# Kernel optimization log

Hardware: AMD Instinct MI355X
Metric: run time of the kernel (lower is better)

The kernel has to match this reference:

```python
import jax, jax.numpy as jnp
import numpy as np

N, F_IN, H, C = 100000, 256, 128, 64
E, EP = 1600000, 500000


def setup_inputs() -> dict:
    key = jax.random.key(0)
    ks = jax.random.split(key, 8)
    x = jax.random.normal(ks[0], (N, F_IN), jnp.float32)
    masked_nodes = jax.random.randint(ks[1], (1000,), 0, N)
    pos_edge_index = jax.random.randint(ks[2], (2, EP), 0, N)
    neg_edge_index = jax.random.randint(ks[3], (2, EP), 0, N)
    edge_index = jax.random.randint(ks[4], (2, E), 0, N)
    W1 = jax.random.normal(ks[5], (F_IN, H), jnp.float32) / np.sqrt(F_IN).astype(np.float32)
    b1 = jnp.zeros((H,), jnp.float32)
    W2 = jax.random.normal(ks[6], (H, C), jnp.float32) / np.sqrt(H).astype(np.float32)
    b2 = jnp.zeros((C,), jnp.float32)
    return dict(x=x, masked_nodes=masked_nodes, pos_edge_index=pos_edge_index,
                neg_edge_index=neg_edge_index, edge_index=edge_index,
                W1=W1, b1=b1, W2=W2, b2=b2)


def gcn_conv(x, W, b, src, dst, n):
    # PyG GCNConv: h = x @ W; symmetric norm with self-loops; aggregate; + bias
    h = x @ W  # [N, out]
    deg = jax.ops.segment_sum(jnp.ones(src.shape[0], h.dtype), dst, num_segments=n) + 1.0
    dis = jax.lax.rsqrt(deg)  # D^{-1/2} including self-loop
    msg = h[src] * (dis[src] * dis[dst])[:, None]           # gather + edge-norm
    agg = jax.ops.segment_sum(msg, dst, num_segments=n)      # scatter-add
    agg = agg + h * (dis * dis)[:, None]                      # self-loop term
    return agg + b


def reference(x, masked_nodes, pos_edge_index, neg_edge_index, edge_index, W1, b1, W2, b2):
    n = x.shape[0]
    src, dst = edge_index[0], edge_index[1]
    h = jax.nn.relu(gcn_conv(x, W1, b1, src, dst, n))
    h = gcn_conv(h, W2, b2, src, dst, n)  # [N, C]
    tei = jnp.concatenate([pos_edge_index, neg_edge_index], axis=-1)  # [2, 2*EP]
    x_j = h[tei[0]]  # [2EP, C]
    x_i = h[tei[1]]
    scores = jnp.einsum('ef,ef->e', x_i, x_j)
    return scores, jnp.zeros(tei.shape, jnp.float32)
```

## Files before the change

kernel.cpp:

```cpp
#include <hip/hip_runtime.h>

#define N_NODES 100000
#define F_IN    256
#define H_DIM   128
#define C_DIM   64
#define E_EDGES 1600000
#define EP_EDGES 500000

#define NBUK 391
#define EPB  4096

typedef unsigned short bf16_t;
typedef short  short8  __attribute__((ext_vector_type(8)));
typedef float  float4v __attribute__((ext_vector_type(4)));
typedef _Float16 half8v __attribute__((ext_vector_type(8)));

__device__ inline bf16_t f2bf(float f) {
    unsigned u = __float_as_uint(f);
    u += 0x7fff + ((u >> 16) & 1);
    return (bf16_t)(u >> 16);
}
__device__ inline float bf2f(bf16_t h) {
    return __uint_as_float(((unsigned)h) << 16);
}
__device__ inline void split8(const float* vv, short* h, short* l) {
#pragma unroll
    for (int j = 0; j < 8; ++j) {
        bf16_t hb = f2bf(vv[j]);
        h[j] = (short)hb;
        l[j] = (short)f2bf(vv[j] - bf2f(hb));
    }
}
__device__ inline float4v mfma16(short8 a, short8 b, float4v c) {
    return __builtin_amdgcn_mfma_f32_16x16x32_bf16(a, b, c, 0, 0, 0);
}
__device__ inline void gload_lds16(const void* gptr, void* lptr) {
    __builtin_amdgcn_global_load_lds(
        (const __attribute__((address_space(1))) unsigned int*)gptr,
        (__attribute__((address_space(3))) unsigned int*)lptr, 16, 0, 0);
}
#define XSWZ(nn) (((nn) >> 1) & 3)

__global__ __launch_bounds__(256) void bhist_kernel(const int* __restrict__ dst,
                                                    int* __restrict__ bsize) {
    __shared__ int hist[NBUK];
    const int t = threadIdx.x;
    for (int b = t; b < NBUK; b += 256) hist[b] = 0;
    __syncthreads();
    const int e0 = blockIdx.x * EPB;
#pragma unroll
    for (int i = 0; i < 16; ++i) {
        int e = e0 + i * 256 + t;
        if (e < E_EDGES) atomicAdd(&hist[dst[e] >> 8], 1);
    }
    __syncthreads();
    for (int b = t; b < NBUK; b += 256)
        if (hist[b]) atomicAdd(&bsize[b], hist[b]);
}

__global__ __launch_bounds__(512) void bscan_kernel(const int* __restrict__ bsize,
                                                    int* __restrict__ bbase,
                                                    int* __restrict__ bcursor) {
    __shared__ int sh[512];
    int t = threadIdx.x;
    sh[t] = (t < NBUK) ? bsize[t] : 0;
    __syncthreads();
#pragma unroll
    for (int off = 1; off < 512; off <<= 1) {
        int u = (t >= off) ? sh[t - off] : 0;
        __syncthreads();
        sh[t] += u;
        __syncthreads();
    }
    if (t < NBUK) {
        int ex = (t == 0) ? 0 : sh[t - 1];
        bbase[t] = ex;
        bcursor[t] = ex;
    }
    if (t == 0) bbase[NBUK] = E_EDGES;
}

__global__ __launch_bounds__(256) void bucket_scatter_kernel(const int* __restrict__ src,
                                                             const int* __restrict__ dst,
                                                             int* __restrict__ bcursor,
                                                             int2* __restrict__ pairs) {
    __shared__ int hist[NBUK];
    __shared__ int base[NBUK];
    const int t = threadIdx.x;
    for (int b = t; b < NBUK; b += 256) hist[b] = 0;
    __syncthreads();

    const int e0 = blockIdx.x * EPB;
    int s[16], d[16];
#pragma unroll
    for (int i = 0; i < 16; ++i) {
        int e = e0 + i * 256 + t;
        if (e < E_EDGES) {
            s[i] = src[e];
            d[i] = dst[e];
            atomicAdd(&hist[d[i] >> 8], 1);
        } else {
            d[i] = -1;
        }
    }
    __syncthreads();
    for (int b = t; b < NBUK; b += 256) {
        int c = hist[b];
        base[b] = c ? atomicAdd(&bcursor[b], c) : 0;
        hist[b] = 0;
    }
    __syncthreads();
#pragma unroll
    for (int i = 0; i < 16; ++i) {
        if (d[i] >= 0) {
            int b = d[i] >> 8;
            int r = atomicAdd(&hist[b], 1);
            pairs[base[b] + r] = make_int2(s[i], d[i]);
        }
    }
}

__global__ __launch_bounds__(256) void bucket_sort_kernel(const int2* __restrict__ pairs,
                                                          const int* __restrict__ bbase,
                                                          int* __restrict__ row_ptr,
                                                          float* __restrict__ dis,
                                                          int* __restrict__ csr_src) {
    __shared__ int cnt[256];
    __shared__ int sh[256];
    __shared__ int cur[256];
    const int b = blockIdx.x;
    const int node0 = b << 8;
    const int t = threadIdx.x;
    const int nn = min(256, N_NODES - node0);
    const int beg = bbase[b], end = bbase[b + 1];
    cnt[t] = 0;
    __syncthreads();
    for (int e = beg + t; e < end; e += 256)
        atomicAdd(&cnt[pairs[e].y - node0], 1);
    __syncthreads();
    int c = cnt[t];
    if (t < nn) dis[node0 + t] = rsqrtf((float)c + 1.0f);
    sh[t] = c;
    __syncthreads();
#pragma unroll
    for (int off = 1; off < 256; off <<= 1) {
        int u = (t >= off) ? sh[t - off] : 0;
        __syncthreads();
        sh[t] += u;
        __syncthreads();
    }
    int start = beg + sh[t] - c;
    if (t < nn) row_ptr[node0 + t] = start;
    cur[t] = start;
    if (b == NBUK - 1 && t == 0) row_ptr[N_NODES] = E_EDGES;
    __syncthreads();
    for (int e = beg + t; e < end; e += 256) {
        int2 p = pairs[e];
        int j = atomicAdd(&cur[p.y - node0], 1);
        csr_src[j] = p.x;
    }
}

__global__ __launch_bounds__(256) void wprep_kernel(const float* __restrict__ W1,
                                                    const float* __restrict__ W2,
                                                    short* __restrict__ w1h,
                                                    short* __restrict__ w1l,
                                                    short* __restrict__ w2h,
                                                    short* __restrict__ w2l) {
    int idx = blockIdx.x * 256 + threadIdx.x;
    if (idx < H_DIM * F_IN) {
        int n = idx >> 8, k = idx & 255;
        int kc = (k >> 3) & 3;
        int dk = (k & ~0x18) | (((kc ^ XSWZ(n)) & 3) << 3);
        float w = W1[k * H_DIM + n];
        bf16_t h = f2bf(w);
        w1h[n * F_IN + dk] = (short)h;
        w1l[n * F_IN + dk] = (short)f2bf(w - bf2f(h));
    }
    int i2 = idx - H_DIM * F_IN;
    if (i2 >= 0 && i2 < C_DIM * H_DIM) {
        int n = i2 >> 7, k = i2 & 127;
        int kc = (k >> 3) & 3;
        int dk = (k & ~0x18) | (((kc ^ XSWZ(n)) & 3) << 3);
        float w = W2[k * C_DIM + n];
        bf16_t h = f2bf(w);
        w2h[n * H_DIM + dk] = (short)h;
        w2l[n * H_DIM + dk] = (short)f2bf(w - bf2f(h));
    }
}

#define G1_STAGE(BUF, KSN)                                                     \
    for (int i_ = 0; i_ < 2; ++i_) {                                           \
        int e_ = t + i_ * 256;                                                 \
        gload_lds16(&Wth[(e_ >> 2) * F_IN + (KSN) * 32 + (e_ & 3) * 8],        \
                    &Bh[(BUF) * 4096 + e_ * 8]);                               \
        gload_lds16(&Wtl[(e_ >> 2) * F_IN + (KSN) * 32 + (e_ & 3) * 8],        \
                    &Bl[(BUF) * 4096 + e_ * 8]);                               \
    }

#define G1_LOADA(BANK, KSN)                                                    \
    if (ok0) {                                                                 \
        *(float4*)&aP[BANK][0][0] = *(const float4*)&X0[(KSN) * 32];           \
        *(float4*)&aP[BANK][0][4] = *(const float4*)&X0[(KSN) * 32 + 4];       \
    }                                                                          \
    if (ok1) {                                                                 \
        *(float4*)&aP[BANK][1][0] = *(const float4*)&X1[(KSN) * 32];           \
        *(float4*)&aP[BANK][1][4] = *(const float4*)&X1[(KSN) * 32 + 4];       \
    }

__global__ __launch_bounds__(256, 3) void gemm1_mfma(const float* __restrict__ X,
                                                     const short* __restrict__ Wth,
                                                     const short* __restrict__ Wtl,
                                                     const float* __restrict__ dis,
                                                     bf16_t* __restrict__ T,
                                                     int nrows) {
    __shared__ short Bh[2 * 4096], Bl[2 * 4096];
    const int t = threadIdx.x;
    const int row0 = blockIdx.x * 128;
    const int w = t >> 6;
    const int lane = t & 63;
    const int m = lane & 15;
    const int q = lane >> 4;
    const int qs = ((q ^ XSWZ(m)) & 3) << 3;

    const int r0 = row0 + w * 32 + m;
    const int r1 = r0 + 16;
    const bool ok0 = r0 < nrows;
    const bool ok1 = r1 < nrows;
    const float* X0 = X + (long long)r0 * F_IN + q * 8;
    const float* X1 = X + (long long)r1 * F_IN + q * 8;

    float4v acc[2][8];
#pragma unroll
    for (int i = 0; i < 2; ++i)
#pragma unroll
        for (int j = 0; j < 8; ++j) acc[i][j] = {0.f, 0.f, 0.f, 0.f};

    float aP[2][2][8] = {};

    G1_STAGE(0, 0)
    G1_LOADA(0, 0)
    __syncthreads();

#pragma unroll
    for (int ks = 0; ks < 8; ++ks) {
        const int p = ks & 1;
        if (ks < 7) {
            G1_STAGE(p ^ 1, ks + 1)
            G1_LOADA(p ^ 1, ks + 1)
        }
        short8 ah0, al0, ah1, al1;
        split8(aP[p][0], (short*)&ah0, (short*)&al0);
        split8(aP[p][1], (short*)&ah1, (short*)&al1);
#pragma unroll
        for (int nc = 0; nc < 8; ++nc) {
            const int bo = p * 4096 + (nc * 16 + m) * 32 + qs;
            short8 bh = *(const short8*)&Bh[bo];
            short8 bl = *(const short8*)&Bl[bo];
            acc[0][nc] = mfma16(ah0, bh, acc[0][nc]);
            acc[0][nc] = mfma16(al0, bh, acc[0][nc]);
            acc[0][nc] = mfma16(ah0, bl, acc[0][nc]);
            acc[1][nc] = mfma16(ah1, bh, acc[1][nc]);
            acc[1][nc] = mfma16(al1, bh, acc[1][nc]);
            acc[1][nc] = mfma16(ah1, bl, acc[1][nc]);
        }
        __syncthreads();
    }
    float ds_[2][4];
#pragma unroll
    for (int mt = 0; mt < 2; ++mt)
#pragma unroll
        for (int reg = 0; reg < 4; ++reg) {
            int grow = row0 + w * 32 + mt * 16 + q * 4 + reg;
            ds_[mt][reg] = (grow < nrows) ? dis[grow] : 0.f;
        }
#pragma unroll
    for (int mt = 0; mt < 2; ++mt)
#pragma unroll
        for (int nc = 0; nc < 8; ++nc)
#pragma unroll
            for (int reg = 0; reg < 4; ++reg) {
                int grow = row0 + w * 32 + mt * 16 + q * 4 + reg;
                int gcol = nc * 16 + m;
                if (grow < nrows)
                    T[(long long)grow * H_DIM + gcol] = f2bf(acc[mt][nc][reg] * ds_[mt][reg]);
            }
}

#define G2_STAGE(BUF, KSN)                                                     \
    gload_lds16(&Wth[(t >> 2) * H_DIM + (KSN) * 32 + (t & 3) * 8],             \
                &Bh[(BUF) * 2048 + t * 8]);                                    \
    gload_lds16(&Wtl[(t >> 2) * H_DIM + (KSN) * 32 + (t & 3) * 8],             \
                &Bl[(BUF) * 2048 + t * 8]);

#define G2_LOADA(BANK, KSN)                                                    \
    if (ok0) {                                                                 \
        *(float4*)&aP[BANK][0][0] = *(const float4*)&A0[(KSN) * 32];           \
        *(float4*)&aP[BANK][0][4] = *(const float4*)&A0[(KSN) * 32 + 4];       \
    }                                                                          \
    if (ok1) {                                                                 \
        *(float4*)&aP[BANK][1][0] = *(const float4*)&A1[(KSN) * 32];           \
        *(float4*)&aP[BANK][1][4] = *(const float4*)&A1[(KSN) * 32 + 4];       \
    }

__global__ __launch_bounds__(256, 3) void gemm2_mfma(const float* __restrict__ A,
                                                     const float* __restrict__ b1,
                                                     const short* __restrict__ Wth,
                                                     const short* __restrict__ Wtl,
                                                     const float* __restrict__ dis,
                                                     bf16_t* __restrict__ T,
                                                     int nrows) {
    __shared__ short Bh[2 * 2048], Bl[2 * 2048];
    const int t = threadIdx.x;
    const int row0 = blockIdx.x * 128;
    const int w = t >> 6;
    const int lane = t & 63;
    const int m = lane & 15;
    const int q = lane >> 4;
    const int qs = ((q ^ XSWZ(m)) & 3) << 3;

    const int r0 = row0 + w * 32 + m;
    const int r1 = r0 + 16;
    const bool ok0 = r0 < nrows;
    const bool ok1 = r1 < nrows;
    const float* A0 = A + (long long)r0 * H_DIM + q * 8;
    const float* A1 = A + (long long)r1 * H_DIM + q * 8;
    const float* bp = b1 + q * 8;

    float4v acc[2][4];
#pragma unroll
    for (int i = 0; i < 2; ++i)
#pragma unroll
        for (int j = 0; j < 4; ++j) acc[i][j] = {0.f, 0.f, 0.f, 0.f};

    float aP[2][2][8] = {};

    G2_STAGE(0, 0)
    G2_LOADA(0, 0)
    __syncthreads();

#pragma unroll
    for (int ks = 0; ks < 4; ++ks) {
        const int p = ks & 1;
        if (ks < 3) {
            G2_STAGE(p ^ 1, ks + 1)
            G2_LOADA(p ^ 1, ks + 1)
        }
        float4 bv0 = *(const float4*)&bp[ks * 32];
        float4 bv1 = *(const float4*)&bp[ks * 32 + 4];
        float a0[8], a1[8];
        a0[0] = fmaxf(aP[p][0][0] + bv0.x, 0.f); a0[1] = fmaxf(aP[p][0][1] + bv0.y, 0.f);
        a0[2] = fmaxf(aP[p][0][2] + bv0.z, 0.f); a0[3] = fmaxf(aP[p][0][3] + bv0.w, 0.f);
        a0[4] = fmaxf(aP[p][0][4] + bv1.x, 0.f); a0[5] = fmaxf(aP[p][0][5] + bv1.y, 0.f);
        a0[6] = fmaxf(aP[p][0][6] + bv1.z, 0.f); a0[7] = fmaxf(aP[p][0][7] + bv1.w, 0.f);
        a1[0] = fmaxf(aP[p][1][0] + bv0.x, 0.f); a1[1] = fmaxf(aP[p][1][1] + bv0.y, 0.f);
        a1[2] = fmaxf(aP[p][1][2] + bv0.z, 0.f); a1[3] = fmaxf(aP[p][1][3] + bv0.w, 0.f);
        a1[4] = fmaxf(aP[p][1][4] + bv1.x, 0.f); a1[5] = fmaxf(aP[p][1][5] + bv1.y, 0.f);
        a1[6] = fmaxf(aP[p][1][6] + bv1.z, 0.f); a1[7] = fmaxf(aP[p][1][7] + bv1.w, 0.f);
        short8 ah0, al0, ah1, al1;
        split8(a0, (short*)&ah0, (short*)&al0);
        split8(a1, (short*)&ah1, (short*)&al1);
#pragma unroll
        for (int nc = 0; nc < 4; ++nc) {
            const int bo = p * 2048 + (nc * 16 + m) * 32 + qs;
            short8 bh = *(const short8*)&Bh[bo];
            short8 bl = *(const short8*)&Bl[bo];
            acc[0][nc] = mfma16(ah0, bh, acc[0][nc]);
            acc[0][nc] = mfma16(al0, bh, acc[0][nc]);
            acc[0][nc] = mfma16(ah0, bl, acc[0][nc]);
            acc[1][nc] = mfma16(ah1, bh, acc[1][nc]);
            acc[1][nc] = mfma16(al1, bh, acc[1][nc]);
            acc[1][nc] = mfma16(ah1, bl, acc[1][nc]);
        }
        __syncthreads();
    }
    float ds_[2][4];
#pragma unroll
    for (int mt = 0; mt < 2; ++mt)
#pragma unroll
        for (int reg = 0; reg < 4; ++reg) {
            int grow = row0 + w * 32 + mt * 16 + q * 4 + reg;
            ds_[mt][reg] = (grow < nrows) ? dis[grow] : 0.f;
        }
#pragma unroll
    for (int mt = 0; mt < 2; ++mt)
#pragma unroll
        for (int nc = 0; nc < 4; ++nc)
#pragma unroll
            for (int reg = 0; reg < 4; ++reg) {
                int grow = row0 + w * 32 + mt * 16 + q * 4 + reg;
                int gcol = nc * 16 + m;
                if (grow < nrows)
                    T[(long long)grow * C_DIM + gcol] = f2bf(acc[mt][nc][reg] * ds_[mt][reg]);
            }
}

__device__ inline void add8_bf16(float* acc, uint4 u) {
#pragma unroll
    for (int p = 0; p < 4; ++p) {
        unsigned w = (&u.x)[p];
        acc[2 * p]     += __uint_as_float(w << 16);
        acc[2 * p + 1] += __uint_as_float(w & 0xffff0000u);
    }
}

template <int CS, bool HAS_BIAS, bool F16OUT>
__global__ __launch_bounds__(256) void agg_kernel(const bf16_t* __restrict__ t,
                                                  const float* __restrict__ dis,
                                                  const int* __restrict__ row_ptr,
                                                  const int* __restrict__ csr_src,
                                                  const float* __restrict__ bias,
                                                  float* __restrict__ aggf,
                                                  _Float16* __restrict__ aggh) {
    unsigned idx = blockIdx.x * 256u + threadIdx.x;
    if (idx >= (unsigned)(N_NODES << CS)) return;
    int node = idx >> CS;
    int q = idx & ((1 << CS) - 1);
    const uint4* tv = (const uint4*)t;
    int beg = row_ptr[node], end = row_ptr[node + 1];

    float acc[8];
    {
        uint4 u = tv[idx];
#pragma unroll
        for (int p = 0; p < 4; ++p) {
            unsigned w = (&u.x)[p];
            acc[2 * p]     = __uint_as_float(w << 16);
            acc[2 * p + 1] = __uint_as_float(w & 0xffff0000u);
        }
    }

    int j = beg;
    for (; j + 3 < end; j += 4) {
        int s0 = csr_src[j + 0], s1 = csr_src[j + 1];
        int s2 = csr_src[j + 2], s3 = csr_src[j + 3];
        uint4 u0 = tv[((unsigned)s0 << CS) + q];
        uint4 u1 = tv[((unsigned)s1 << CS) + q];
        uint4 u2 = tv[((unsigned)s2 << CS) + q];
        uint4 u3 = tv[((unsigned)s3 << CS) + q];
        add8_bf16(acc, u0);
        add8_bf16(acc, u1);
        add8_bf16(acc, u2);
        add8_bf16(acc, u3);
    }
    for (; j < end; ++j) {
        int s = csr_src[j];
        add8_bf16(acc, tv[((unsigned)s << CS) + q]);
    }

    float dd = dis[node];
#pragma unroll
    for (int p = 0; p < 8; ++p) acc[p] *= dd;

    if (HAS_BIAS) {
        float4 bv0 = ((const float4*)bias)[q * 2];
        float4 bv1 = ((const float4*)bias)[q * 2 + 1];
        acc[0] += bv0.x; acc[1] += bv0.y; acc[2] += bv0.z; acc[3] += bv0.w;
        acc[4] += bv1.x; acc[5] += bv1.y; acc[6] += bv1.z; acc[7] += bv1.w;
    }
    if (F16OUT) {
        half8v hv;
#pragma unroll
        for (int p = 0; p < 8; ++p) hv[p] = (_Float16)acc[p];
        ((half8v*)aggh)[idx] = hv;
    } else {
        float4 o0 = make_float4(acc[0], acc[1], acc[2], acc[3]);
        float4 o1 = make_float4(acc[4], acc[5], acc[6], acc[7]);
        ((float4*)aggf)[idx * 2]     = o0;
        ((float4*)aggf)[idx * 2 + 1] = o1;
    }
}

__global__ __launch_bounds__(256) void score_kernel(const _Float16* __restrict__ h2,
                                                    const int* __restrict__ pos,
                                                    const int* __restrict__ neg,
                                                    float* __restrict__ out) {
    int tid = blockIdx.x * 256 + threadIdx.x;
    int e = tid >> 3;
    int q = tid & 7;
    if (e >= 2 * EP_EDGES) return;
    int i, j;
    if (e < EP_EDGES) {
        j = pos[e];
        i = pos[EP_EDGES + e];
    } else {
        j = neg[e - EP_EDGES];
        i = neg[e];
    }
    half8v a = ((const half8v*)h2)[i * 8 + q];
    half8v b = ((const half8v*)h2)[j * 8 + q];
    float v = 0.f;
#pragma unroll
    for (int k = 0; k < 8; ++k) v = fmaf((float)a[k], (float)b[k], v);
    v += __shfl_down(v, 4, 8);
    v += __shfl_down(v, 2, 8);
    v += __shfl_down(v, 1, 8);
    if (q == 0) out[e] = v;
}

extern "C" void kernel_launch(void* const* d_in, const int* in_sizes, int n_in,
                              void* d_out, int out_size, void* d_ws, size_t ws_size,
                              hipStream_t stream) {
    const float* x  = (const float*)d_in[0];
    const int* pos  = (const int*)d_in[2];
    const int* neg  = (const int*)d_in[3];
    const int* ei   = (const int*)d_in[4];
    const float* W1 = (const float*)d_in[5];
    const float* b1 = (const float*)d_in[6];
    const float* W2 = (const float*)d_in[7];
    const float* b2 = (const float*)d_in[8];
    float* out = (float*)d_out;

    char* ws = (char*)d_ws;
    float*  dis     = (float*) (ws + 0);
    int*    row_ptr = (int*)   (ws + 400000);
    int*    bsize   = (int*)   (ws + 800128);
    int*    bbase   = (int*)   (ws + 801792);
    int*    bcursor = (int*)   (ws + 803456);
    int*    csr_src = (int*)   (ws + 805120);
    int2*   pairs   = (int2*)  (ws + 7205120);
    _Float16* h2f16 = (_Float16*)(ws + 7205120);
    bf16_t* t       = (bf16_t*)(ws + 20005120);
    float*  agg     = (float*) (ws + 45605120);
    short*  w1th    = (short*) (ws + 96805120);
    short*  w1tl    = (short*) (ws + 96870656);
    short*  w2th    = (short*) (ws + 96936192);
    short*  w2tl    = (short*) (ws + 96952576);

    const int* esrc = ei;
    const int* edst = ei + E_EDGES;

    hipMemsetAsync(bsize, 0, NBUK * sizeof(int), stream);
    bhist_kernel<<<(E_EDGES + EPB - 1) / EPB, 256, 0, stream>>>(edst, bsize);
    bscan_kernel<<<1, 512, 0, stream>>>(bsize, bbase, bcursor);
    bucket_scatter_kernel<<<(E_EDGES + EPB - 1) / EPB, 256, 0, stream>>>(
        esrc, edst, bcursor, pairs);
    bucket_sort_kernel<<<NBUK, 256, 0, stream>>>(pairs, bbase, row_ptr, dis, csr_src);
    wprep_kernel<<<(H_DIM * F_IN + C_DIM * H_DIM + 255) / 256, 256, 0, stream>>>(
        W1, W2, w1th, w1tl, w2th, w2tl);

    gemm1_mfma<<<(N_NODES + 127) / 128, 256, 0, stream>>>(x, w1th, w1tl, dis, t, N_NODES);
    agg_kernel<4, false, false><<<(N_NODES * 16 + 255) / 256, 256, 0, stream>>>(
        t, dis, row_ptr, csr_src, nullptr, agg, nullptr);

    gemm2_mfma<<<(N_NODES + 127) / 128, 256, 0, stream>>>(agg, b1, w2th, w2tl, dis, t, N_NODES);
    agg_kernel<3, true, true><<<(N_NODES * 8 + 255) / 256, 256, 0, stream>>>(
        t, dis, row_ptr, csr_src, b2, nullptr, h2f16);

    score_kernel<<<(2 * EP_EDGES * 8) / 256, 256, 0, stream>>>(h2f16, pos, neg, out);

    hipMemsetAsync(out + 2 * EP_EDGES, 0, (size_t)4 * EP_EDGES * sizeof(float), stream);
}
```

Measured before the change: 400.3 us.

## Pack bucket pairs into 32-bit words and use 512-thread gemm1 blocks

Bucket scatter now packs the source index and the low 8 bits of the destination into one 32-bit word instead of an int2. This halves the traffic for writing and reading pairs in the sort kernel. gemm1 now runs 512 threads per block, with each wave computing a 16-row tile instead of 32. That halves the accumulator and A-operand registers per thread to allow more resident waves, at the cost of less B-tile reuse per wave.

```diff
diff --git a/kernel.cpp b/kernel.cpp
--- a/kernel.cpp
+++ b/kernel.cpp
@@ -83,7 +83,7 @@
 __global__ __launch_bounds__(256) void bucket_scatter_kernel(const int* __restrict__ src,
                                                              const int* __restrict__ dst,
                                                              int* __restrict__ bcursor,
-                                                             int2* __restrict__ pairs) {
+                                                             unsigned* __restrict__ pairs) {
     __shared__ int hist[NBUK];
     __shared__ int base[NBUK];
     const int t = threadIdx.x;
@@ -115,12 +115,12 @@
         if (d[i] >= 0) {
             int b = d[i] >> 8;
             int r = atomicAdd(&hist[b], 1);
-            pairs[base[b] + r] = make_int2(s[i], d[i]);
-        }
-    }
-}
-
-__global__ __launch_bounds__(256) void bucket_sort_kernel(const int2* __restrict__ pairs,
+            pairs[base[b] + r] = ((unsigned)(d[i] & 255) << 24) | (unsigned)s[i];
+        }
+    }
+}
+
+__global__ __launch_bounds__(256) void bucket_sort_kernel(const unsigned* __restrict__ pairs,
                                                           const int* __restrict__ bbase,
                                                           int* __restrict__ row_ptr,
                                                           float* __restrict__ dis,
@@ -136,7 +136,7 @@
     cnt[t] = 0;
     __syncthreads();
     for (int e = beg + t; e < end; e += 256)
-        atomicAdd(&cnt[pairs[e].y - node0], 1);
+        atomicAdd(&cnt[pairs[e] >> 24], 1);
     __syncthreads();
     int c = cnt[t];
     if (t < nn) dis[node0 + t] = rsqrtf((float)c + 1.0f);
@@ -155,9 +155,9 @@
     if (b == NBUK - 1 && t == 0) row_ptr[N_NODES] = E_EDGES;
     __syncthreads();
     for (int e = beg + t; e < end; e += 256) {
-        int2 p = pairs[e];
-        int j = atomicAdd(&cur[p.y - node0], 1);
-        csr_src[j] = p.x;
+        unsigned p = pairs[e];
+        int j = atomicAdd(&cur[p >> 24], 1);
+        csr_src[j] = (int)(p & 0xFFFFFFu);
     }
 }
 
@@ -190,31 +190,24 @@
 }
 
 #define G1_STAGE(BUF, KSN)                                                     \
-    for (int i_ = 0; i_ < 2; ++i_) {                                           \
-        int e_ = t + i_ * 256;                                                 \
-        gload_lds16(&Wth[(e_ >> 2) * F_IN + (KSN) * 32 + (e_ & 3) * 8],        \
-                    &Bh[(BUF) * 4096 + e_ * 8]);                               \
-        gload_lds16(&Wtl[(e_ >> 2) * F_IN + (KSN) * 32 + (e_ & 3) * 8],        \
-                    &Bl[(BUF) * 4096 + e_ * 8]);                               \
-    }
+    gload_lds16(&Wth[(t >> 2) * F_IN + (KSN) * 32 + (t & 3) * 8],              \
+                &SB[(BUF) * 4096 + t * 8]);                                    \
+    gload_lds16(&Wtl[(t >> 2) * F_IN + (KSN) * 32 + (t & 3) * 8],              \
+                &SB[8192 + (BUF) * 4096 + t * 8]);
 
 #define G1_LOADA(BANK, KSN)                                                    \
     if (ok0) {                                                                 \
-        *(float4*)&aP[BANK][0][0] = *(const float4*)&X0[(KSN) * 32];           \
-        *(float4*)&aP[BANK][0][4] = *(const float4*)&X0[(KSN) * 32 + 4];       \
-    }                                                                          \
-    if (ok1) {                                                                 \
-        *(float4*)&aP[BANK][1][0] = *(const float4*)&X1[(KSN) * 32];           \
-        *(float4*)&aP[BANK][1][4] = *(const float4*)&X1[(KSN) * 32 + 4];       \
-    }
-
-__global__ __launch_bounds__(256, 3) void gemm1_mfma(const float* __restrict__ X,
+        *(float4*)&aP[BANK][0] = *(const float4*)&X0[(KSN) * 32];              \
+        *(float4*)&aP[BANK][4] = *(const float4*)&X0[(KSN) * 32 + 4];          \
+    }
+
+__global__ __launch_bounds__(512, 6) void gemm1_mfma(const float* __restrict__ X,
                                                      const short* __restrict__ Wth,
                                                      const short* __restrict__ Wtl,
                                                      const float* __restrict__ dis,
                                                      bf16_t* __restrict__ T,
                                                      int nrows) {
-    __shared__ short Bh[2 * 4096], Bl[2 * 4096];
+    __shared__ short SB[16384];
     const int t = threadIdx.x;
     const int row0 = blockIdx.x * 128;
     const int w = t >> 6;
@@ -223,20 +216,15 @@
     const int q = lane >> 4;
     const int qs = ((q ^ XSWZ(m)) & 3) << 3;
 
-    const int r0 = row0 + w * 32 + m;
-    const int r1 = r0 + 16;
+    const int r0 = row0 + w * 16 + m;
     const bool ok0 = r0 < nrows;
-    const bool ok1 = r1 < nrows;
     const float* X0 = X + (long long)r0 * F_IN + q * 8;
-    const float* X1 = X + (long long)r1 * F_IN + q * 8;
-
-    float4v acc[2][8];
-#pragma unroll
-    for (int i = 0; i < 2; ++i)
-#pragma unroll
-        for (int j = 0; j < 8; ++j) acc[i][j] = {0.f, 0.f, 0.f, 0.f};
-
-    float aP[2][2][8] = {};
+
+    float4v acc[8];
+#pragma unroll
+    for (int j = 0; j < 8; ++j) acc[j] = {0.f, 0.f, 0.f, 0.f};
+
+    float aP[2][8] = {};
 
     G1_STAGE(0, 0)
     G1_LOADA(0, 0)
@@ -249,42 +237,34 @@
             G1_STAGE(p ^ 1, ks + 1)
             G1_LOADA(p ^ 1, ks + 1)
         }
-        short8 ah0, al0, ah1, al1;
-        split8(aP[p][0], (short*)&ah0, (short*)&al0);
-        split8(aP[p][1], (short*)&ah1, (short*)&al1);
+        short8 ah0, al0;
+        split8(aP[p], (short*)&ah0, (short*)&al0);
 #pragma unroll
         for (int nc = 0; nc < 8; ++nc) {
             const int bo = p * 4096 + (nc * 16 + m) * 32 + qs;
-            short8 bh = *(const short8*)&Bh[bo];
-            short8 bl = *(const short8*)&Bl[bo];
-            acc[0][nc] = mfma16(ah0, bh, acc[0][nc]);
-            acc[0][nc] = mfma16(al0, bh, acc[0][nc]);
-            acc[0][nc] = mfma16(ah0, bl, acc[0][nc]);
-            acc[1][nc] = mfma16(ah1, bh, acc[1][nc]);
-            acc[1][nc] = mfma16(al1, bh, acc[1][nc]);
-            acc[1][nc] = mfma16(ah1, bl, acc[1][nc]);
+            short8 bh = *(const short8*)&SB[bo];
+            short8 bl = *(const short8*)&SB[8192 + bo];
+            acc[nc] = mfma16(ah0, bh, acc[nc]);
+            acc[nc] = mfma16(al0, bh, acc[nc]);
+            acc[nc] = mfma16(ah0, bl, acc[nc]);
         }
         __syncthreads();
     }
-    float ds_[2][4];
-#pragma unroll
-    for (int mt = 0; mt < 2; ++mt)
+    float ds_[4];
+#pragma unroll
+    for (int reg = 0; reg < 4; ++reg) {
+        int grow = row0 + w * 16 + q * 4 + reg;
+        ds_[reg] = (grow < nrows) ? dis[grow] : 0.f;
+    }
+#pragma unroll
+    for (int nc = 0; nc < 8; ++nc)
 #pragma unroll
         for (int reg = 0; reg < 4; ++reg) {
-            int grow = row0 + w * 32 + mt * 16 + q * 4 + reg;
-            ds_[mt][reg] = (grow < nrows) ? dis[grow] : 0.f;
-        }
-#pragma unroll
-    for (int mt = 0; mt < 2; ++mt)
-#pragma unroll
-        for (int nc = 0; nc < 8; ++nc)
-#pragma unroll
-            for (int reg = 0; reg < 4; ++reg) {
-                int grow = row0 + w * 32 + mt * 16 + q * 4 + reg;
-                int gcol = nc * 16 + m;
-                if (grow < nrows)
-                    T[(long long)grow * H_DIM + gcol] = f2bf(acc[mt][nc][reg] * ds_[mt][reg]);
-            }
+            int grow = row0 + w * 16 + q * 4 + reg;
+            int gcol = nc * 16 + m;
+            if (grow < nrows)
+                T[(long long)grow * H_DIM + gcol] = f2bf(acc[nc][reg] * ds_[reg]);
+        }
 }
 
 #define G2_STAGE(BUF, KSN)                                                     \
@@ -518,7 +498,7 @@
     int*    bbase   = (int*)   (ws + 801792);
     int*    bcursor = (int*)   (ws + 803456);
     int*    csr_src = (int*)   (ws + 805120);
-    int2*   pairs   = (int2*)  (ws + 7205120);
+    unsigned* pairs = (unsigned*)(ws + 7205120);
     _Float16* h2f16 = (_Float16*)(ws + 7205120);
     bf16_t* t       = (bf16_t*)(ws + 20005120);
     float*  agg     = (float*) (ws + 45605120);
@@ -539,7 +519,7 @@
     wprep_kernel<<<(H_DIM * F_IN + C_DIM * H_DIM + 255) / 256, 256, 0, stream>>>(
         W1, W2, w1th, w1tl, w2th, w2tl);
 
-    gemm1_mfma<<<(N_NODES + 127) / 128, 256, 0, stream>>>(x, w1th, w1tl, dis, t, N_NODES);
+    gemm1_mfma<<<(N_NODES + 127) / 128, 512, 0, stream>>>(x, w1th, w1tl, dis, t, N_NODES);
     agg_kernel<4, false, false><<<(N_NODES * 16 + 255) / 256, 256, 0, stream>>>(
         t, dis, row_ptr, csr_src, nullptr, agg, nullptr);
 
```

Result: no change. 404.4 us (+1.0%).

## Pack bucket pairs into 32-bit words and restage GEMM loads in bulk phases

Applied to the files above, without the earlier changes.

Bucket scatter now stores each edge as one 32-bit word, with the local destination in the high 8 bits and the source in the low 24 bits. This halves the traffic for writing and reading the intermediate pairs array. gemm1 switches from a per-k-step double buffer to two bulk phases: it loads half of the weights and all of the X row fragments into registers up front, which cuts barriers and lets more loads be in flight. In exchange it uses more LDS and registers, and launch bounds drop to 2 blocks per SM. gemm2 likewise loads all weights and A fragments before computing, with a single barrier.

```diff
diff --git a/kernel.cpp b/kernel.cpp
--- a/kernel.cpp
+++ b/kernel.cpp
@@ -83,7 +83,7 @@
 __global__ __launch_bounds__(256) void bucket_scatter_kernel(const int* __restrict__ src,
                                                              const int* __restrict__ dst,
                                                              int* __restrict__ bcursor,
-                                                             int2* __restrict__ pairs) {
+                                                             unsigned* __restrict__ pairs) {
     __shared__ int hist[NBUK];
     __shared__ int base[NBUK];
     const int t = threadIdx.x;
@@ -115,12 +115,12 @@
         if (d[i] >= 0) {
             int b = d[i] >> 8;
             int r = atomicAdd(&hist[b], 1);
-            pairs[base[b] + r] = make_int2(s[i], d[i]);
-        }
-    }
-}
-
-__global__ __launch_bounds__(256) void bucket_sort_kernel(const int2* __restrict__ pairs,
+            pairs[base[b] + r] = ((unsigned)(d[i] & 255) << 24) | (unsigned)s[i];
+        }
+    }
+}
+
+__global__ __launch_bounds__(256) void bucket_sort_kernel(const unsigned* __restrict__ pairs,
                                                           const int* __restrict__ bbase,
                                                           int* __restrict__ row_ptr,
                                                           float* __restrict__ dis,
@@ -136,7 +136,7 @@
     cnt[t] = 0;
     __syncthreads();
     for (int e = beg + t; e < end; e += 256)
-        atomicAdd(&cnt[pairs[e].y - node0], 1);
+        atomicAdd(&cnt[pairs[e] >> 24], 1);
     __syncthreads();
     int c = cnt[t];
     if (t < nn) dis[node0 + t] = rsqrtf((float)c + 1.0f);
@@ -155,9 +155,9 @@
     if (b == NBUK - 1 && t == 0) row_ptr[N_NODES] = E_EDGES;
     __syncthreads();
     for (int e = beg + t; e < end; e += 256) {
-        int2 p = pairs[e];
-        int j = atomicAdd(&cur[p.y - node0], 1);
-        csr_src[j] = p.x;
+        unsigned p = pairs[e];
+        int j = atomicAdd(&cur[p >> 24], 1);
+        csr_src[j] = (int)(p & 0xFFFFFFu);
     }
 }
 
@@ -189,32 +189,13 @@
     }
 }
 
-#define G1_STAGE(BUF, KSN)                                                     \
-    for (int i_ = 0; i_ < 2; ++i_) {                                           \
-        int e_ = t + i_ * 256;                                                 \
-        gload_lds16(&Wth[(e_ >> 2) * F_IN + (KSN) * 32 + (e_ & 3) * 8],        \
-                    &Bh[(BUF) * 4096 + e_ * 8]);                               \
-        gload_lds16(&Wtl[(e_ >> 2) * F_IN + (KSN) * 32 + (e_ & 3) * 8],        \
-                    &Bl[(BUF) * 4096 + e_ * 8]);                               \
-    }
-
-#define G1_LOADA(BANK, KSN)                                                    \
-    if (ok0) {                                                                 \
-        *(float4*)&aP[BANK][0][0] = *(const float4*)&X0[(KSN) * 32];           \
-        *(float4*)&aP[BANK][0][4] = *(const float4*)&X0[(KSN) * 32 + 4];       \
-    }                                                                          \
-    if (ok1) {                                                                 \
-        *(float4*)&aP[BANK][1][0] = *(const float4*)&X1[(KSN) * 32];           \
-        *(float4*)&aP[BANK][1][4] = *(const float4*)&X1[(KSN) * 32 + 4];       \
-    }
-
-__global__ __launch_bounds__(256, 3) void gemm1_mfma(const float* __restrict__ X,
+__global__ __launch_bounds__(256, 2) void gemm1_mfma(const float* __restrict__ X,
                                                      const short* __restrict__ Wth,
                                                      const short* __restrict__ Wtl,
                                                      const float* __restrict__ dis,
                                                      bf16_t* __restrict__ T,
                                                      int nrows) {
-    __shared__ short Bh[2 * 4096], Bl[2 * 4096];
+    __shared__ short SB[32768];
     const int t = threadIdx.x;
     const int row0 = blockIdx.x * 128;
     const int w = t >> 6;
@@ -236,25 +217,182 @@
 #pragma unroll
         for (int j = 0; j < 8; ++j) acc[i][j] = {0.f, 0.f, 0.f, 0.f};
 
-    float aP[2][2][8] = {};
-
-    G1_STAGE(0, 0)
-    G1_LOADA(0, 0)
-    __syncthreads();
-
-#pragma unroll
-    for (int ks = 0; ks < 8; ++ks) {
-        const int p = ks & 1;
-        if (ks < 7) {
-            G1_STAGE(p ^ 1, ks + 1)
-            G1_LOADA(p ^ 1, ks + 1)
-        }
+    float aP[4][2][8] = {};
+    float aQ[4][2][8] = {};
+
+#pragma unroll
+    for (int pp = 0; pp < 4; ++pp)
+#pragma unroll
+        for (int i_ = 0; i_ < 2; ++i_) {
+            int e_ = t + i_ * 256;
+            gload_lds16(&Wth[(e_ >> 2) * F_IN + pp * 32 + (e_ & 3) * 8],
+                        &SB[pp * 4096 + e_ * 8]);
+            gload_lds16(&Wtl[(e_ >> 2) * F_IN + pp * 32 + (e_ & 3) * 8],
+                        &SB[16384 + pp * 4096 + e_ * 8]);
+        }
+    if (ok0)
+#pragma unroll
+        for (int pp = 0; pp < 4; ++pp) {
+            *(float4*)&aP[pp][0][0] = *(const float4*)&X0[pp * 32];
+            *(float4*)&aP[pp][0][4] = *(const float4*)&X0[pp * 32 + 4];
+            *(float4*)&aQ[pp][0][0] = *(const float4*)&X0[(pp + 4) * 32];
+            *(float4*)&aQ[pp][0][4] = *(const float4*)&X0[(pp + 4) * 32 + 4];
+        }
+    if (ok1)
+#pragma unroll
+        for (int pp = 0; pp < 4; ++pp) {
+            *(float4*)&aP[pp][1][0] = *(const float4*)&X1[pp * 32];
+            *(float4*)&aP[pp][1][4] = *(const float4*)&X1[pp * 32 + 4];
+            *(float4*)&aQ[pp][1][0] = *(const float4*)&X1[(pp + 4) * 32];
+            *(float4*)&aQ[pp][1][4] = *(const float4*)&X1[(pp + 4) * 32 + 4];
+        }
+    __syncthreads();
+
+#pragma unroll
+    for (int pp = 0; pp < 4; ++pp) {
         short8 ah0, al0, ah1, al1;
-        split8(aP[p][0], (short*)&ah0, (short*)&al0);
-        split8(aP[p][1], (short*)&ah1, (short*)&al1);
+        split8(aP[pp][0], (short*)&ah0, (short*)&al0);
+        split8(aP[pp][1], (short*)&ah1, (short*)&al1);
 #pragma unroll
         for (int nc = 0; nc < 8; ++nc) {
-            const int bo = p * 4096 + (nc * 16 + m) * 32 + qs;
+            const int bo = pp * 4096 + (nc * 16 + m) * 32 + qs;
+            short8 bh = *(const short8*)&SB[bo];
+            short8 bl = *(const short8*)&SB[16384 + bo];
+            acc[0][nc] = mfma16(ah0, bh, acc[0][nc]);
+            acc[0][nc] = mfma16(al0, bh, acc[0][nc]);
+            acc[0][nc] = mfma16(ah0, bl, acc[0][nc]);
+            acc[1][nc] = mfma16(ah1, bh, acc[1][nc]);
+            acc[1][nc] = mfma16(al1, bh, acc[1][nc]);
+            acc[1][nc] = mfma16(ah1, bl, acc[1][nc]);
+        }
+    }
+    __syncthreads();
+
+#pragma unroll
+    for (int pp = 0; pp < 4; ++pp)
+#pragma unroll
+        for (int i_ = 0; i_ < 2; ++i_) {
+            int e_ = t + i_ * 256;
+            gload_lds16(&Wth[(e_ >> 2) * F_IN + (pp + 4) * 32 + (e_ & 3) * 8],
+                        &SB[pp * 4096 + e_ * 8]);
+            gload_lds16(&Wtl[(e_ >> 2) * F_IN + (pp + 4) * 32 + (e_ & 3) * 8],
+                        &SB[16384 + pp * 4096 + e_ * 8]);
+        }
+    __syncthreads();
+
+#pragma unroll
+    for (int pp = 0; pp < 4; ++pp) {
+        short8 ah0, al0, ah1, al1;
+        split8(aQ[pp][0], (short*)&ah0, (short*)&al0);
+        split8(aQ[pp][1], (short*)&ah1, (short*)&al1);
+#pragma unroll
+        for (int nc = 0; nc < 8; ++nc) {
+            const int bo = pp * 4096 + (nc * 16 + m) * 32 + qs;
+            short8 bh = *(const short8*)&SB[bo];
+            short8 bl = *(const short8*)&SB[16384 + bo];
+            acc[0][nc] = mfma16(ah0, bh, acc[0][nc]);
+            acc[0][nc] = mfma16(al0, bh, acc[0][nc]);
+            acc[0][nc] = mfma16(ah0, bl, acc[0][nc]);
+            acc[1][nc] = mfma16(ah1, bh, acc[1][nc]);
+            acc[1][nc] = mfma16(al1, bh, acc[1][nc]);
+            acc[1][nc] = mfma16(ah1, bl, acc[1][nc]);
+        }
+    }
+
+    float ds_[2][4];
+#pragma unroll
+    for (int mt = 0; mt < 2; ++mt)
+#pragma unroll
+        for (int reg = 0; reg < 4; ++reg) {
+            int grow = row0 + w * 32 + mt * 16 + q * 4 + reg;
+            ds_[mt][reg] = (grow < nrows) ? dis[grow] : 0.f;
+        }
+#pragma unroll
+    for (int mt = 0; mt < 2; ++mt)
+#pragma unroll
+        for (int nc = 0; nc < 8; ++nc)
+#pragma unroll
+            for (int reg = 0; reg < 4; ++reg) {
+                int grow = row0 + w * 32 + mt * 16 + q * 4 + reg;
+                int gcol = nc * 16 + m;
+                if (grow < nrows)
+                    T[(long long)grow * H_DIM + gcol] = f2bf(acc[mt][nc][reg] * ds_[mt][reg]);
+            }
+}
+
+__global__ __launch_bounds__(256) void gemm2_mfma(const float* __restrict__ A,
+                                                  const float* __restrict__ b1,
+                                                  const short* __restrict__ Wth,
+                                                  const short* __restrict__ Wtl,
+                                                  const float* __restrict__ dis,
+                                                  bf16_t* __restrict__ T,
+                                                  int nrows) {
+    __shared__ short Bh[4 * 2048], Bl[4 * 2048];
+    const int t = threadIdx.x;
+    const int row0 = blockIdx.x * 128;
+    const int w = t >> 6;
+    const int lane = t & 63;
+    const int m = lane & 15;
+    const int q = lane >> 4;
+    const int qs = ((q ^ XSWZ(m)) & 3) << 3;
+
+    const int r0 = row0 + w * 32 + m;
+    const int r1 = r0 + 16;
+    const bool ok0 = r0 < nrows;
+    const bool ok1 = r1 < nrows;
+    const float* A0 = A + (long long)r0 * H_DIM + q * 8;
+    const float* A1 = A + (long long)r1 * H_DIM + q * 8;
+    const float* bp = b1 + q * 8;
+
+#pragma unroll
+    for (int ks = 0; ks < 4; ++ks) {
+        gload_lds16(&Wth[(t >> 2) * H_DIM + ks * 32 + (t & 3) * 8],
+                    &Bh[ks * 2048 + t * 8]);
+        gload_lds16(&Wtl[(t >> 2) * H_DIM + ks * 32 + (t & 3) * 8],
+                    &Bl[ks * 2048 + t * 8]);
+    }
+    float aP[4][2][8] = {};
+    if (ok0) {
+#pragma unroll
+        for (int ks = 0; ks < 4; ++ks) {
+            *(float4*)&aP[ks][0][0] = *(const float4*)&A0[ks * 32];
+            *(float4*)&aP[ks][0][4] = *(const float4*)&A0[ks * 32 + 4];
+        }
+    }
+    if (ok1) {
+#pragma unroll
+        for (int ks = 0; ks < 4; ++ks) {
+            *(float4*)&aP[ks][1][0] = *(const float4*)&A1[ks * 32];
+            *(float4*)&aP[ks][1][4] = *(const float4*)&A1[ks * 32 + 4];
+        }
+    }
+    __syncthreads();
+
+    float4v acc[2][4];
+#pragma unroll
+    for (int i = 0; i < 2; ++i)
+#pragma unroll
+        for (int j = 0; j < 4; ++j) acc[i][j] = {0.f, 0.f, 0.f, 0.f};
+
+#pragma unroll
+    for (int ks = 0; ks < 4; ++ks) {
+        float4 bv0 = *(const float4*)&bp[ks * 32];
+        float4 bv1 = *(const float4*)&bp[ks * 32 + 4];
+        float a0[8], a1[8];
+        a0[0] = fmaxf(aP[ks][0][0] + bv0.x, 0.f); a0[1] = fmaxf(aP[ks][0][1] + bv0.y, 0.f);
+        a0[2] = fmaxf(aP[ks][0][2] + bv0.z, 0.f); a0[3] = fmaxf(aP[ks][0][3] + bv0.w, 0.f);
+        a0[4] = fmaxf(aP[ks][0][4] + bv1.x, 0.f); a0[5] = fmaxf(aP[ks][0][5] + bv1.y, 0.f);
+        a0[6] = fmaxf(aP[ks][0][6] + bv1.z, 0.f); a0[7] = fmaxf(aP[ks][0][7] + bv1.w, 0.f);
+        a1[0] = fmaxf(aP[ks][1][0] + bv0.x, 0.f); a1[1] = fmaxf(aP[ks][1][1] + bv0.y, 0.f);
+        a1[2] = fmaxf(aP[ks][1][2] + bv0.z, 0.f); a1[3] = fmaxf(aP[ks][1][3] + bv0.w, 0.f);
+        a1[4] = fmaxf(aP[ks][1][4] + bv1.x, 0.f); a1[5] = fmaxf(aP[ks][1][5] + bv1.y, 0.f);
+        a1[6] = fmaxf(aP[ks][1][6] + bv1.z, 0.f); a1[7] = fmaxf(aP[ks][1][7] + bv1.w, 0.f);
+        short8 ah0, al0, ah1, al1;
+        split8(a0, (short*)&ah0, (short*)&al0);
+        split8(a1, (short*)&ah1, (short*)&al1);
+#pragma unroll
+        for (int nc = 0; nc < 4; ++nc) {
+            const int bo = ks * 2048 + (nc * 16 + m) * 32 + qs;
             short8 bh = *(const short8*)&Bh[bo];
             short8 bl = *(const short8*)&Bl[bo];
             acc[0][nc] = mfma16(ah0, bh, acc[0][nc]);
@@ -264,115 +402,6 @@
             acc[1][nc] = mfma16(al1, bh, acc[1][nc]);
             acc[1][nc] = mfma16(ah1, bl, acc[1][nc]);
         }
-        __syncthreads();
-    }
-    float ds_[2][4];
-#pragma unroll
-    for (int mt = 0; mt < 2; ++mt)
-#pragma unroll
-        for (int reg = 0; reg < 4; ++reg) {
-            int grow = row0 + w * 32 + mt * 16 + q * 4 + reg;
-            ds_[mt][reg] = (grow < nrows) ? dis[grow] : 0.f;
-        }
-#pragma unroll
-    for (int mt = 0; mt < 2; ++mt)
-#pragma unroll
-        for (int nc = 0; nc < 8; ++nc)
-#pragma unroll
-            for (int reg = 0; reg < 4; ++reg) {
-                int grow = row0 + w * 32 + mt * 16 + q * 4 + reg;
-                int gcol = nc * 16 + m;
-                if (grow < nrows)
-                    T[(long long)grow * H_DIM + gcol] = f2bf(acc[mt][nc][reg] * ds_[mt][reg]);
-            }
-}
-
-#define G2_STAGE(BUF, KSN)                                                     \
-    gload_lds16(&Wth[(t >> 2) * H_DIM + (KSN) * 32 + (t & 3) * 8],             \
-                &Bh[(BUF) * 2048 + t * 8]);                                    \
-    gload_lds16(&Wtl[(t >> 2) * H_DIM + (KSN) * 32 + (t & 3) * 8],             \
-                &Bl[(BUF) * 2048 + t * 8]);
-
-#define G2_LOADA(BANK, KSN)                                                    \
-    if (ok0) {                                                                 \
-        *(float4*)&aP[BANK][0][0] = *(const float4*)&A0[(KSN) * 32];           \
-        *(float4*)&aP[BANK][0][4] = *(const float4*)&A0[(KSN) * 32 + 4];       \
-    }                                                                          \
-    if (ok1) {                                                                 \
-        *(float4*)&aP[BANK][1][0] = *(const float4*)&A1[(KSN) * 32];           \
-        *(float4*)&aP[BANK][1][4] = *(const float4*)&A1[(KSN) * 32 + 4];       \
-    }
-
-__global__ __launch_bounds__(256, 3) void gemm2_mfma(const float* __restrict__ A,
-                                                     const float* __restrict__ b1,
-                                                     const short* __restrict__ Wth,
-                                                     const short* __restrict__ Wtl,
-                                                     const float* __restrict__ dis,
-                                                     bf16_t* __restrict__ T,
-                                                     int nrows) {
-    __shared__ short Bh[2 * 2048], Bl[2 * 2048];
-    const int t = threadIdx.x;
-    const int row0 = blockIdx.x * 128;
-    const int w = t >> 6;
-    const int lane = t & 63;
-    const int m = lane & 15;
-    const int q = lane >> 4;
-    const int qs = ((q ^ XSWZ(m)) & 3) << 3;
-
-    const int r0 = row0 + w * 32 + m;
-    const int r1 = r0 + 16;
-    const bool ok0 = r0 < nrows;
-    const bool ok1 = r1 < nrows;
-    const float* A0 = A + (long long)r0 * H_DIM + q * 8;
-    const float* A1 = A + (long long)r1 * H_DIM + q * 8;
-    const float* bp = b1 + q * 8;
-
-    float4v acc[2][4];
-#pragma unroll
-    for (int i = 0; i < 2; ++i)
-#pragma unroll
-        for (int j = 0; j < 4; ++j) acc[i][j] = {0.f, 0.f, 0.f, 0.f};
-
-    float aP[2][2][8] = {};
-
-    G2_STAGE(0, 0)
-    G2_LOADA(0, 0)
-    __syncthreads();
-
-#pragma unroll
-    for (int ks = 0; ks < 4; ++ks) {
-        const int p = ks & 1;
-        if (ks < 3) {
-            G2_STAGE(p ^ 1, ks + 1)
-            G2_LOADA(p ^ 1, ks + 1)
-        }
-        float4 bv0 = *(const float4*)&bp[ks * 32];
-        float4 bv1 = *(const float4*)&bp[ks * 32 + 4];
-        float a0[8], a1[8];
-        a0[0] = fmaxf(aP[p][0][0] + bv0.x, 0.f); a0[1] = fmaxf(aP[p][0][1] + bv0.y, 0.f);
-        a0[2] = fmaxf(aP[p][0][2] + bv0.z, 0.f); a0[3] = fmaxf(aP[p][0][3] + bv0.w, 0.f);
-        a0[4] = fmaxf(aP[p][0][4] + bv1.x, 0.f); a0[5] = fmaxf(aP[p][0][5] + bv1.y, 0.f);
-        a0[6] = fmaxf(aP[p][0][6] + bv1.z, 0.f); a0[7] = fmaxf(aP[p][0][7] + bv1.w, 0.f);
-        a1[0] = fmaxf(aP[p][1][0] + bv0.x, 0.f); a1[1] = fmaxf(aP[p][1][1] + bv0.y, 0.f);
-        a1[2] = fmaxf(aP[p][1][2] + bv0.z, 0.f); a1[3] = fmaxf(aP[p][1][3] + bv0.w, 0.f);
-        a1[4] = fmaxf(aP[p][1][4] + bv1.x, 0.f); a1[5] = fmaxf(aP[p][1][5] + bv1.y, 0.f);
-        a1[6] = fmaxf(aP[p][1][6] + bv1.z, 0.f); a1[7] = fmaxf(aP[p][1][7] + bv1.w, 0.f);
-        short8 ah0, al0, ah1, al1;
-        split8(a0, (short*)&ah0, (short*)&al0);
-        split8(a1, (short*)&ah1, (short*)&al1);
-#pragma unroll
-        for (int nc = 0; nc < 4; ++nc) {
-            const int bo = p * 2048 + (nc * 16 + m) * 32 + qs;
-            short8 bh = *(const short8*)&Bh[bo];
-            short8 bl = *(const short8*)&Bl[bo];
-            acc[0][nc] = mfma16(ah0, bh, acc[0][nc]);
-            acc[0][nc] = mfma16(al0, bh, acc[0][nc]);
-            acc[0][nc] = mfma16(ah0, bl, acc[0][nc]);
-            acc[1][nc] = mfma16(ah1, bh, acc[1][nc]);
-            acc[1][nc] = mfma16(al1, bh, acc[1][nc]);
-            acc[1][nc] = mfma16(ah1, bl, acc[1][nc]);
-        }
-        __syncthreads();
     }
     float ds_[2][4];
 #pragma unroll
@@ -518,7 +547,7 @@
     int*    bbase   = (int*)   (ws + 801792);
     int*    bcursor = (int*)   (ws + 803456);
     int*    csr_src = (int*)   (ws + 805120);
-    int2*   pairs   = (int2*)  (ws + 7205120);
+    unsigned* pairs = (unsigned*)(ws + 7205120);
     _Float16* h2f16 = (_Float16*)(ws + 7205120);
     bf16_t* t       = (bf16_t*)(ws + 20005120);
     float*  agg     = (float*) (ws + 45605120);
```

After: 409.4 us. 1.02x slower.
